# Optimization experiments

Hardware: AMD Instinct MI355X
Metric: run time of the kernel (lower is better)

The kernel has to match this reference:

```python
import jax, jax.numpy as jnp
import numpy as np

B, S, D, F_DIM, E, TOPK = 2, 1024, 1024, 4096, 8, 2


def setup_inputs() -> dict:
    key = jax.random.key(0)
    k0, k1, k2, k3 = jax.random.split(key, 4)
    hidden_states = jax.random.normal(k0, (B, S, D), dtype=jnp.float32)
    # torch nn.Linear stores weight as [out_features, in_features]
    router_w = jax.random.normal(k1, (E, D), dtype=jnp.float32) * 0.02
    w1 = jax.random.normal(k2, (E, F_DIM, D), dtype=jnp.float32) * 0.02
    w2 = jax.random.normal(k3, (E, D, F_DIM), dtype=jnp.float32) * 0.02
    expert_scale = jnp.ones((E,), dtype=jnp.float32)
    return {"hidden_states": hidden_states, "router_w": router_w,
            "w1": w1, "w2": w2, "expert_scale": expert_scale}


def reference(hidden_states, router_w, w1, w2, expert_scale):
    b, s, d = hidden_states.shape
    xf = hidden_states.reshape(-1, d)                      # [T, D]
    logits = xf @ router_w.T                               # [T, E]
    probs = jax.nn.softmax(logits, axis=-1)
    top_w, top_idx = jax.lax.top_k(probs, TOPK)            # [T, K]
    top_w = jax.nn.softmax(top_w, axis=-1)                 # renormalize over top-k
    # Combine weights per expert: sum of slot weights routed to each expert. [T, E]
    combine = jnp.sum(jax.nn.one_hot(top_idx, E, dtype=xf.dtype) * top_w[..., None], axis=1)
    # Dense per-expert SiLU MLP for all tokens (grouped GEMM form).
    h = jax.nn.silu(jnp.einsum('td,efd->tef', xf, w1))     # [T, E, F]
    y = jnp.einsum('tef,edf->ted', h, w2)                  # [T, E, D]
    y = y * expert_scale[None, :, None]
    out = jnp.einsum('te,ted->td', combine, y)             # [T, D]
    return out.reshape(b, s, d)
```

## Files before the change

kernel.cpp:

```cpp
#include <hip/hip_runtime.h>
#include <hip/hip_bf16.h>
#include <stdint.h>

#define NT 2048
#define DD 1024
#define FF 4096
#define NE 8
#define NSLOT (NT*2)

typedef float  f32x4  __attribute__((ext_vector_type(4)));
typedef __bf16 bf16x8 __attribute__((ext_vector_type(8)));
typedef __bf16 bf16x4 __attribute__((ext_vector_type(4)));

__global__ void k_convert_x(const float* __restrict__ x, __bf16* __restrict__ xb) {
    int i = blockIdx.x * blockDim.x + threadIdx.x;
    float4 v = reinterpret_cast<const float4*>(x)[i];
    bf16x4 o;
    o[0] = (__bf16)v.x; o[1] = (__bf16)v.y; o[2] = (__bf16)v.z; o[3] = (__bf16)v.w;
    reinterpret_cast<bf16x4*>(xb)[i] = o;
}

__global__ void k_router(const float* __restrict__ x, const float* __restrict__ rw,
                         const float* __restrict__ escale,
                         int* __restrict__ counts, int* __restrict__ rank,
                         int* __restrict__ tidx, float* __restrict__ tw) {
    int t = blockIdx.x;
    int lane = threadIdx.x;
    const float* xr = x + (size_t)t * DD + lane * 16;
    float acc[NE];
    #pragma unroll
    for (int e = 0; e < NE; e++) acc[e] = 0.f;
    #pragma unroll
    for (int c = 0; c < 4; c++) {
        float4 xv = reinterpret_cast<const float4*>(xr)[c];
        #pragma unroll
        for (int e = 0; e < NE; e++) {
            float4 rv = reinterpret_cast<const float4*>(rw + (size_t)e * DD + lane * 16)[c];
            acc[e] += xv.x*rv.x + xv.y*rv.y + xv.z*rv.z + xv.w*rv.w;
        }
    }
    #pragma unroll
    for (int e = 0; e < NE; e++) {
        #pragma unroll
        for (int off = 32; off > 0; off >>= 1) acc[e] += __shfl_xor(acc[e], off);
    }
    if (lane == 0) {
        int e0 = 0; float l0 = acc[0];
        #pragma unroll
        for (int e = 1; e < NE; e++) if (acc[e] > l0) { l0 = acc[e]; e0 = e; }
        int e1 = (e0 == 0) ? 1 : 0; float l1 = acc[e1];
        #pragma unroll
        for (int e = 0; e < NE; e++) if (e != e0 && acc[e] > l1) { l1 = acc[e]; e1 = e; }
        float sum = 0.f;
        #pragma unroll
        for (int e = 0; e < NE; e++) sum += __expf(acc[e] - l0);
        float p0 = 1.0f / sum;
        float p1 = __expf(l1 - l0) / sum;
        float z  = __expf(p1 - p0);
        float w0 = 1.0f / (1.0f + z);
        float w1 = 1.0f - w0;
        tidx[t*2+0] = e0; tw[t*2+0] = w0 * escale[e0];
        tidx[t*2+1] = e1; tw[t*2+1] = w1 * escale[e1];
        rank[t*2+0] = atomicAdd(&counts[e0], 1);
        rank[t*2+1] = atomicAdd(&counts[e1], 1);
    }
}

__global__ void k_prefix(const int* __restrict__ counts, int* __restrict__ offsets) {
    if (threadIdx.x == 0) {
        int s = 0;
        for (int e = 0; e < NE; e++) { offsets[e] = s; s += counts[e]; }
        offsets[NE] = s;
    }
}

__global__ void k_scatter(const int* __restrict__ tidx, const float* __restrict__ tw,
                          const int* __restrict__ rank, const int* __restrict__ offsets,
                          int* __restrict__ slot_token, int* __restrict__ slot_k,
                          float* __restrict__ slot_w) {
    int t = blockIdx.x * blockDim.x + threadIdx.x;
    if (t >= NT) return;
    #pragma unroll
    for (int k = 0; k < 2; k++) {
        int e = tidx[t*2+k];
        int p = offsets[e] + rank[t*2+k];
        slot_token[p] = t; slot_k[p] = k; slot_w[p] = tw[t*2+k];
    }
}

#define BM 128
#define BN 128
#define BK 32
#define LDT 40

__launch_bounds__(256)
__global__ void k_gemm1(const __bf16* __restrict__ xb, const float* __restrict__ w1,
                        const int* __restrict__ offsets, const int* __restrict__ slot_token,
                        __bf16* __restrict__ H) {
    int e = blockIdx.z;
    int base = offsets[e];
    int Me = offsets[e+1] - base;
    int m0 = blockIdx.x * BM;
    if (m0 >= Me) return;
    int n0 = blockIdx.y * BN;

    __shared__ __bf16 As[BM][LDT];
    __shared__ __bf16 Bs[BN][LDT];

    int tid = threadIdx.x;
    int wave = tid >> 6, lane = tid & 63;
    int wm = (wave & 1) * 64, wn = (wave >> 1) * 64;

    int arow = tid >> 1, ahalf = tid & 1;
    int rloc = min(m0 + arow, Me - 1);
    int tok  = slot_token[base + rloc];
    const __bf16* aptr = xb + (size_t)tok * DD + ahalf * 16;
    const float*  bptr = w1 + ((size_t)e * FF + n0 + arow) * DD + ahalf * 16;

    f32x4 zero4 = {0.f, 0.f, 0.f, 0.f};
    f32x4 acc[4][4];
    #pragma unroll
    for (int m = 0; m < 4; m++)
        #pragma unroll
        for (int n = 0; n < 4; n++) acc[m][n] = zero4;

    for (int k0 = 0; k0 < DD; k0 += BK) {
        const bf16x8* ap = reinterpret_cast<const bf16x8*>(aptr + k0);
        bf16x8 a0 = ap[0], a1 = ap[1];
        const float4* bp = reinterpret_cast<const float4*>(bptr + k0);
        float4 q0 = bp[0], q1 = bp[1], q2 = bp[2], q3 = bp[3];
        bf16x8 b0, b1;
        b0[0]=(__bf16)q0.x; b0[1]=(__bf16)q0.y; b0[2]=(__bf16)q0.z; b0[3]=(__bf16)q0.w;
        b0[4]=(__bf16)q1.x; b0[5]=(__bf16)q1.y; b0[6]=(__bf16)q1.z; b0[7]=(__bf16)q1.w;
        b1[0]=(__bf16)q2.x; b1[1]=(__bf16)q2.y; b1[2]=(__bf16)q2.z; b1[3]=(__bf16)q2.w;
        b1[4]=(__bf16)q3.x; b1[5]=(__bf16)q3.y; b1[6]=(__bf16)q3.z; b1[7]=(__bf16)q3.w;
        *reinterpret_cast<bf16x8*>(&As[arow][ahalf*16    ]) = a0;
        *reinterpret_cast<bf16x8*>(&As[arow][ahalf*16 + 8]) = a1;
        *reinterpret_cast<bf16x8*>(&Bs[arow][ahalf*16    ]) = b0;
        *reinterpret_cast<bf16x8*>(&Bs[arow][ahalf*16 + 8]) = b1;
        __syncthreads();
        bf16x8 af[4], bfr[4];
        #pragma unroll
        for (int m = 0; m < 4; m++)
            af[m] = *reinterpret_cast<const bf16x8*>(&As[wm + m*16 + (lane & 15)][(lane >> 4) * 8]);
        #pragma unroll
        for (int n = 0; n < 4; n++)
            bfr[n] = *reinterpret_cast<const bf16x8*>(&Bs[wn + n*16 + (lane & 15)][(lane >> 4) * 8]);
        #pragma unroll
        for (int m = 0; m < 4; m++)
            #pragma unroll
            for (int n = 0; n < 4; n++)
                acc[m][n] = __builtin_amdgcn_mfma_f32_16x16x32_bf16(af[m], bfr[n], acc[m][n], 0, 0, 0);
        __syncthreads();
    }

    int rbase = wm + (lane >> 4) * 4;
    int cbase = n0 + wn + (lane & 15);
    #pragma unroll
    for (int m = 0; m < 4; m++) {
        #pragma unroll
        for (int j = 0; j < 4; j++) {
            int rl = m0 + rbase + m*16 + j;
            if (rl < Me) {
                #pragma unroll
                for (int n = 0; n < 4; n++) {
                    float v = acc[m][n][j];
                    float s = v / (1.0f + __expf(-v));
                    H[(size_t)(base + rl) * FF + cbase + n*16] = (__bf16)s;
                }
            }
        }
    }
}

__launch_bounds__(256)
__global__ void k_gemm2(const __bf16* __restrict__ H, const float* __restrict__ w2,
                        const int* __restrict__ offsets,
                        const int* __restrict__ slot_token, const int* __restrict__ slot_k,
                        const float* __restrict__ slot_w,
                        float* __restrict__ ybuf) {
    int e = blockIdx.z;
    int base = offsets[e];
    int Me = offsets[e+1] - base;
    int m0 = blockIdx.x * BM;
    if (m0 >= Me) return;
    int n0 = blockIdx.y * BN;

    __shared__ __bf16 As[BM][LDT];
    __shared__ __bf16 Bs[BN][LDT];

    int tid = threadIdx.x;
    int wave = tid >> 6, lane = tid & 63;
    int wm = (wave & 1) * 64, wn = (wave >> 1) * 64;

    int arow = tid >> 1, ahalf = tid & 1;
    int rloc = min(m0 + arow, Me - 1);
    const __bf16* aptr = H  + (size_t)(base + rloc) * FF + ahalf * 16;
    const float*  bptr = w2 + ((size_t)e * DD + n0 + arow) * FF + ahalf * 16;

    f32x4 zero4 = {0.f, 0.f, 0.f, 0.f};
    f32x4 acc[4][4];
    #pragma unroll
    for (int m = 0; m < 4; m++)
        #pragma unroll
        for (int n = 0; n < 4; n++) acc[m][n] = zero4;

    for (int k0 = 0; k0 < FF; k0 += BK) {
        const bf16x8* ap = reinterpret_cast<const bf16x8*>(aptr + k0);
        bf16x8 a0 = ap[0], a1 = ap[1];
        const float4* bp = reinterpret_cast<const float4*>(bptr + k0);
        float4 q0 = bp[0], q1 = bp[1], q2 = bp[2], q3 = bp[3];
        bf16x8 b0, b1;
        b0[0]=(__bf16)q0.x; b0[1]=(__bf16)q0.y; b0[2]=(__bf16)q0.z; b0[3]=(__bf16)q0.w;
        b0[4]=(__bf16)q1.x; b0[5]=(__bf16)q1.y; b0[6]=(__bf16)q1.z; b0[7]=(__bf16)q1.w;
        b1[0]=(__bf16)q2.x; b1[1]=(__bf16)q2.y; b1[2]=(__bf16)q2.z; b1[3]=(__bf16)q2.w;
        b1[4]=(__bf16)q3.x; b1[5]=(__bf16)q3.y; b1[6]=(__bf16)q3.z; b1[7]=(__bf16)q3.w;
        *reinterpret_cast<bf16x8*>(&As[arow][ahalf*16    ]) = a0;
        *reinterpret_cast<bf16x8*>(&As[arow][ahalf*16 + 8]) = a1;
        *reinterpret_cast<bf16x8*>(&Bs[arow][ahalf*16    ]) = b0;
        *reinterpret_cast<bf16x8*>(&Bs[arow][ahalf*16 + 8]) = b1;
        __syncthreads();
        bf16x8 af[4], bfr[4];
        #pragma unroll
        for (int m = 0; m < 4; m++)
            af[m] = *reinterpret_cast<const bf16x8*>(&As[wm + m*16 + (lane & 15)][(lane >> 4) * 8]);
        #pragma unroll
        for (int n = 0; n < 4; n++)
            bfr[n] = *reinterpret_cast<const bf16x8*>(&Bs[wn + n*16 + (lane & 15)][(lane >> 4) * 8]);
        #pragma unroll
        for (int m = 0; m < 4; m++)
            #pragma unroll
            for (int n = 0; n < 4; n++)
                acc[m][n] = __builtin_amdgcn_mfma_f32_16x16x32_bf16(af[m], bfr[n], acc[m][n], 0, 0, 0);
        __syncthreads();
    }

    int rbase = wm + (lane >> 4) * 4;
    int cb = n0 + wn + (lane & 15);
    #pragma unroll
    for (int m = 0; m < 4; m++) {
        #pragma unroll
        for (int j = 0; j < 4; j++) {
            int rl = m0 + rbase + m*16 + j;
            if (rl < Me) {
                int p = base + rl;
                int tok = slot_token[p];
                int kk  = slot_k[p];
                float wv = slot_w[p];
                float* yrow = ybuf + ((size_t)tok * 2 + kk) * DD + cb;
                #pragma unroll
                for (int n = 0; n < 4; n++) yrow[n*16] = acc[m][n][j] * wv;
            }
        }
    }
}

__global__ void k_combine(const float* __restrict__ yb, float* __restrict__ out) {
    int i = blockIdx.x * blockDim.x + threadIdx.x;
    int t = i >> 8;
    int c = i & 255;
    const f32x4* a = reinterpret_cast<const f32x4*>(yb + (size_t)t * 2 * DD);
    f32x4 va = a[c];
    f32x4 vb = a[c + 256];
    reinterpret_cast<f32x4*>(out)[i] = va + vb;
}

extern "C" void kernel_launch(void* const* d_in, const int* in_sizes, int n_in,
                              void* d_out, int out_size, void* d_ws, size_t ws_size,
                              hipStream_t stream) {
    const float* x  = (const float*)d_in[0];
    const float* rw = (const float*)d_in[1];
    const float* w1 = (const float*)d_in[2];
    const float* w2 = (const float*)d_in[3];
    const float* es = (const float*)d_in[4];
    float* out = (float*)d_out;

    uint8_t* ws = (uint8_t*)d_ws;
    __bf16* xb   = (__bf16*)ws;  ws += (size_t)NT * DD * 2;
    __bf16* H    = (__bf16*)ws;  ws += (size_t)NSLOT * FF * 2;
    float*  ybuf = (float*)ws;   ws += (size_t)NT * 2 * DD * 4;
    int*    counts   = (int*)ws; ws += 64;
    int*    offsets  = (int*)ws; ws += 64;
    int*    tidx     = (int*)ws; ws += (size_t)NT * 2 * 4;
    float*  tw       = (float*)ws; ws += (size_t)NT * 2 * 4;
    int*    rank     = (int*)ws; ws += (size_t)NT * 2 * 4;
    int*    slot_token = (int*)ws; ws += (size_t)NSLOT * 4;
    int*    slot_k     = (int*)ws; ws += (size_t)NSLOT * 4;
    float*  slot_w     = (float*)ws; ws += (size_t)NSLOT * 4;

    hipMemsetAsync(counts, 0, NE * sizeof(int), stream);
    k_convert_x<<<NT * DD / 4 / 256, 256, 0, stream>>>(x, xb);
    k_router<<<NT, 64, 0, stream>>>(x, rw, es, counts, rank, tidx, tw);
    k_prefix<<<1, 1, 0, stream>>>(counts, offsets);
    k_scatter<<<NT / 256, 256, 0, stream>>>(tidx, tw, rank, offsets, slot_token, slot_k, slot_w);
    dim3 g1(NT / BM, FF / BN, NE);
    k_gemm1<<<g1, 256, 0, stream>>>(xb, w1, offsets, slot_token, H);
    dim3 g2(NT / BM, DD / BN, NE);
    k_gemm2<<<g2, 256, 0, stream>>>(H, w2, offsets, slot_token, slot_k, slot_w, ybuf);
    k_combine<<<NT * DD / 4 / 256, 256, 0, stream>>>(ybuf, out);
}
```

Before: 938.9 us.

## Use direct global-to-LDS loads, split-K second GEMM with atomic combine, fuse x conversion

Both grouped GEMMs now stage tiles with global_load_lds straight into shared memory, keeping the fp32 weights in LDS and converting them to bf16 when building fragments. The second GEMM is split along K into four chunks and accumulates the weighted results into the zeroed output with atomicAdd, which removes the ybuf intermediate and the combine kernel. The x-to-bf16 conversion is folded into the router kernel. In exchange, LDS traffic grows because fp32 B tiles are twice as large, atomic contention rises, and the floating-point sum order becomes nondeterministic.

```diff
diff --git a/kernel.cpp b/kernel.cpp
--- a/kernel.cpp
+++ b/kernel.cpp
@@ -12,31 +12,38 @@
 typedef __bf16 bf16x8 __attribute__((ext_vector_type(8)));
 typedef __bf16 bf16x4 __attribute__((ext_vector_type(4)));
 
-__global__ void k_convert_x(const float* __restrict__ x, __bf16* __restrict__ xb) {
-    int i = blockIdx.x * blockDim.x + threadIdx.x;
-    float4 v = reinterpret_cast<const float4*>(x)[i];
-    bf16x4 o;
-    o[0] = (__bf16)v.x; o[1] = (__bf16)v.y; o[2] = (__bf16)v.z; o[3] = (__bf16)v.w;
-    reinterpret_cast<bf16x4*>(xb)[i] = o;
+__device__ __forceinline__ void gl16(void* lds, const void* g) {
+    __builtin_amdgcn_global_load_lds(
+        (const __attribute__((address_space(1))) void*)g,
+        (__attribute__((address_space(3))) void*)lds, 16, 0, 0);
 }
 
 __global__ void k_router(const float* __restrict__ x, const float* __restrict__ rw,
-                         const float* __restrict__ escale,
+                         const float* __restrict__ escale, __bf16* __restrict__ xb,
                          int* __restrict__ counts, int* __restrict__ rank,
                          int* __restrict__ tidx, float* __restrict__ tw) {
     int t = blockIdx.x;
     int lane = threadIdx.x;
     const float* xr = x + (size_t)t * DD + lane * 16;
+    float4 xv[4];
+    #pragma unroll
+    for (int c = 0; c < 4; c++) xv[c] = reinterpret_cast<const float4*>(xr)[c];
+    #pragma unroll
+    for (int c = 0; c < 4; c++) {
+        bf16x4 o;
+        o[0] = (__bf16)xv[c].x; o[1] = (__bf16)xv[c].y;
+        o[2] = (__bf16)xv[c].z; o[3] = (__bf16)xv[c].w;
+        *reinterpret_cast<bf16x4*>(xb + (size_t)t * DD + lane * 16 + c * 4) = o;
+    }
     float acc[NE];
     #pragma unroll
     for (int e = 0; e < NE; e++) acc[e] = 0.f;
     #pragma unroll
     for (int c = 0; c < 4; c++) {
-        float4 xv = reinterpret_cast<const float4*>(xr)[c];
         #pragma unroll
         for (int e = 0; e < NE; e++) {
             float4 rv = reinterpret_cast<const float4*>(rw + (size_t)e * DD + lane * 16)[c];
-            acc[e] += xv.x*rv.x + xv.y*rv.y + xv.z*rv.z + xv.w*rv.w;
+            acc[e] += xv[c].x*rv.x + xv[c].y*rv.y + xv[c].z*rv.z + xv[c].w*rv.w;
         }
     }
     #pragma unroll
@@ -76,22 +83,21 @@
 
 __global__ void k_scatter(const int* __restrict__ tidx, const float* __restrict__ tw,
                           const int* __restrict__ rank, const int* __restrict__ offsets,
-                          int* __restrict__ slot_token, int* __restrict__ slot_k,
-                          float* __restrict__ slot_w) {
+                          int* __restrict__ slot_token, float* __restrict__ slot_w) {
     int t = blockIdx.x * blockDim.x + threadIdx.x;
     if (t >= NT) return;
     #pragma unroll
     for (int k = 0; k < 2; k++) {
         int e = tidx[t*2+k];
         int p = offsets[e] + rank[t*2+k];
-        slot_token[p] = t; slot_k[p] = k; slot_w[p] = tw[t*2+k];
+        slot_token[p] = t; slot_w[p] = tw[t*2+k];
     }
 }
 
 #define BM 128
 #define BN 128
 #define BK 32
-#define LDT 40
+#define KSPLIT 4
 
 __launch_bounds__(256)
 __global__ void k_gemm1(const __bf16* __restrict__ xb, const float* __restrict__ w1,
@@ -104,48 +110,53 @@
     if (m0 >= Me) return;
     int n0 = blockIdx.y * BN;
 
-    __shared__ __bf16 As[BM][LDT];
-    __shared__ __bf16 Bs[BN][LDT];
-
-    int tid = threadIdx.x;
-    int wave = tid >> 6, lane = tid & 63;
+    __shared__ __bf16 As[BM*BK];
+    __shared__ float  Bs[BN*BK];
+
+    int tid = threadIdx.x, wave = tid >> 6, lane = tid & 63;
     int wm = (wave & 1) * 64, wn = (wave >> 1) * 64;
 
-    int arow = tid >> 1, ahalf = tid & 1;
-    int rloc = min(m0 + arow, Me - 1);
-    int tok  = slot_token[base + rloc];
-    const __bf16* aptr = xb + (size_t)tok * DD + ahalf * 16;
-    const float*  bptr = w1 + ((size_t)e * FF + n0 + arow) * DD + ahalf * 16;
-
-    f32x4 zero4 = {0.f, 0.f, 0.f, 0.f};
+    const __bf16* aptr[2];
+    #pragma unroll
+    for (int j = 0; j < 2; j++) {
+        int r = (wave*2 + j) * 16 + (lane >> 2);
+        int rl = min(m0 + r, Me - 1);
+        int tok = slot_token[base + rl];
+        aptr[j] = xb + (size_t)tok * DD + (lane & 3) * 8;
+    }
+    const float* bptr[4];
+    #pragma unroll
+    for (int j = 0; j < 4; j++) {
+        int r = (wave*4 + j) * 8 + (lane >> 3);
+        bptr[j] = w1 + ((size_t)e * FF + n0 + r) * DD + (lane & 7) * 4;
+    }
+
     f32x4 acc[4][4];
     #pragma unroll
     for (int m = 0; m < 4; m++)
         #pragma unroll
-        for (int n = 0; n < 4; n++) acc[m][n] = zero4;
+        for (int n = 0; n < 4; n++) acc[m][n] = (f32x4){0.f,0.f,0.f,0.f};
 
     for (int k0 = 0; k0 < DD; k0 += BK) {
-        const bf16x8* ap = reinterpret_cast<const bf16x8*>(aptr + k0);
-        bf16x8 a0 = ap[0], a1 = ap[1];
-        const float4* bp = reinterpret_cast<const float4*>(bptr + k0);
-        float4 q0 = bp[0], q1 = bp[1], q2 = bp[2], q3 = bp[3];
-        bf16x8 b0, b1;
-        b0[0]=(__bf16)q0.x; b0[1]=(__bf16)q0.y; b0[2]=(__bf16)q0.z; b0[3]=(__bf16)q0.w;
-        b0[4]=(__bf16)q1.x; b0[5]=(__bf16)q1.y; b0[6]=(__bf16)q1.z; b0[7]=(__bf16)q1.w;
-        b1[0]=(__bf16)q2.x; b1[1]=(__bf16)q2.y; b1[2]=(__bf16)q2.z; b1[3]=(__bf16)q2.w;
-        b1[4]=(__bf16)q3.x; b1[5]=(__bf16)q3.y; b1[6]=(__bf16)q3.z; b1[7]=(__bf16)q3.w;
-        *reinterpret_cast<bf16x8*>(&As[arow][ahalf*16    ]) = a0;
-        *reinterpret_cast<bf16x8*>(&As[arow][ahalf*16 + 8]) = a1;
-        *reinterpret_cast<bf16x8*>(&Bs[arow][ahalf*16    ]) = b0;
-        *reinterpret_cast<bf16x8*>(&Bs[arow][ahalf*16 + 8]) = b1;
+        #pragma unroll
+        for (int j = 0; j < 2; j++) gl16(&As[(wave*2 + j) * 512], aptr[j] + k0);
+        #pragma unroll
+        for (int j = 0; j < 4; j++) gl16(&Bs[(wave*4 + j) * 256], bptr[j] + k0);
         __syncthreads();
         bf16x8 af[4], bfr[4];
         #pragma unroll
         for (int m = 0; m < 4; m++)
-            af[m] = *reinterpret_cast<const bf16x8*>(&As[wm + m*16 + (lane & 15)][(lane >> 4) * 8]);
-        #pragma unroll
-        for (int n = 0; n < 4; n++)
-            bfr[n] = *reinterpret_cast<const bf16x8*>(&Bs[wn + n*16 + (lane & 15)][(lane >> 4) * 8]);
+            af[m] = *reinterpret_cast<const bf16x8*>(&As[(wm + m*16 + (lane & 15)) * BK + (lane >> 4) * 8]);
+        #pragma unroll
+        for (int n = 0; n < 4; n++) {
+            const float* p = &Bs[(wn + n*16 + (lane & 15)) * BK + (lane >> 4) * 8];
+            float4 x0 = *reinterpret_cast<const float4*>(p);
+            float4 x1 = *reinterpret_cast<const float4*>(p + 4);
+            bf16x8 t;
+            t[0]=(__bf16)x0.x; t[1]=(__bf16)x0.y; t[2]=(__bf16)x0.z; t[3]=(__bf16)x0.w;
+            t[4]=(__bf16)x1.x; t[5]=(__bf16)x1.y; t[6]=(__bf16)x1.z; t[7]=(__bf16)x1.w;
+            bfr[n] = t;
+        }
         #pragma unroll
         for (int m = 0; m < 4; m++)
             #pragma unroll
@@ -176,57 +187,65 @@
 __launch_bounds__(256)
 __global__ void k_gemm2(const __bf16* __restrict__ H, const float* __restrict__ w2,
                         const int* __restrict__ offsets,
-                        const int* __restrict__ slot_token, const int* __restrict__ slot_k,
-                        const float* __restrict__ slot_w,
-                        float* __restrict__ ybuf) {
+                        const int* __restrict__ slot_token, const float* __restrict__ slot_w,
+                        float* __restrict__ out) {
     int e = blockIdx.z;
     int base = offsets[e];
     int Me = offsets[e+1] - base;
-    int m0 = blockIdx.x * BM;
+    int mt = blockIdx.x & 15;
+    int ch = blockIdx.x >> 4;
+    int m0 = mt * BM;
     if (m0 >= Me) return;
     int n0 = blockIdx.y * BN;
-
-    __shared__ __bf16 As[BM][LDT];
-    __shared__ __bf16 Bs[BN][LDT];
-
-    int tid = threadIdx.x;
-    int wave = tid >> 6, lane = tid & 63;
+    const int KCH = FF / KSPLIT;
+    int kbeg = ch * KCH;
+
+    __shared__ __bf16 As[BM*BK];
+    __shared__ float  Bs[BN*BK];
+
+    int tid = threadIdx.x, wave = tid >> 6, lane = tid & 63;
     int wm = (wave & 1) * 64, wn = (wave >> 1) * 64;
 
-    int arow = tid >> 1, ahalf = tid & 1;
-    int rloc = min(m0 + arow, Me - 1);
-    const __bf16* aptr = H  + (size_t)(base + rloc) * FF + ahalf * 16;
-    const float*  bptr = w2 + ((size_t)e * DD + n0 + arow) * FF + ahalf * 16;
-
-    f32x4 zero4 = {0.f, 0.f, 0.f, 0.f};
+    const __bf16* aptr[2];
+    #pragma unroll
+    for (int j = 0; j < 2; j++) {
+        int r = (wave*2 + j) * 16 + (lane >> 2);
+        int rl = min(m0 + r, Me - 1);
+        aptr[j] = H + (size_t)(base + rl) * FF + kbeg + (lane & 3) * 8;
+    }
+    const float* bptr[4];
+    #pragma unroll
+    for (int j = 0; j < 4; j++) {
+        int r = (wave*4 + j) * 8 + (lane >> 3);
+        bptr[j] = w2 + ((size_t)e * DD + n0 + r) * FF + kbeg + (lane & 7) * 4;
+    }
+
     f32x4 acc[4][4];
     #pragma unroll
     for (int m = 0; m < 4; m++)
         #pragma unroll
-        for (int n = 0; n < 4; n++) acc[m][n] = zero4;
-
-    for (int k0 = 0; k0 < FF; k0 += BK) {
-        const bf16x8* ap = reinterpret_cast<const bf16x8*>(aptr + k0);
-        bf16x8 a0 = ap[0], a1 = ap[1];
-        const float4* bp = reinterpret_cast<const float4*>(bptr + k0);
-        float4 q0 = bp[0], q1 = bp[1], q2 = bp[2], q3 = bp[3];
-        bf16x8 b0, b1;
-        b0[0]=(__bf16)q0.x; b0[1]=(__bf16)q0.y; b0[2]=(__bf16)q0.z; b0[3]=(__bf16)q0.w;
-        b0[4]=(__bf16)q1.x; b0[5]=(__bf16)q1.y; b0[6]=(__bf16)q1.z; b0[7]=(__bf16)q1.w;
-        b1[0]=(__bf16)q2.x; b1[1]=(__bf16)q2.y; b1[2]=(__bf16)q2.z; b1[3]=(__bf16)q2.w;
-        b1[4]=(__bf16)q3.x; b1[5]=(__bf16)q3.y; b1[6]=(__bf16)q3.z; b1[7]=(__bf16)q3.w;
-        *reinterpret_cast<bf16x8*>(&As[arow][ahalf*16    ]) = a0;
-        *reinterpret_cast<bf16x8*>(&As[arow][ahalf*16 + 8]) = a1;
-        *reinterpret_cast<bf16x8*>(&Bs[arow][ahalf*16    ]) = b0;
-        *reinterpret_cast<bf16x8*>(&Bs[arow][ahalf*16 + 8]) = b1;
+        for (int n = 0; n < 4; n++) acc[m][n] = (f32x4){0.f,0.f,0.f,0.f};
+
+    for (int k0 = 0; k0 < KCH; k0 += BK) {
+        #pragma unroll
+        for (int j = 0; j < 2; j++) gl16(&As[(wave*2 + j) * 512], aptr[j] + k0);
+        #pragma unroll
+        for (int j = 0; j < 4; j++) gl16(&Bs[(wave*4 + j) * 256], bptr[j] + k0);
         __syncthreads();
         bf16x8 af[4], bfr[4];
         #pragma unroll
         for (int m = 0; m < 4; m++)
-            af[m] = *reinterpret_cast<const bf16x8*>(&As[wm + m*16 + (lane & 15)][(lane >> 4) * 8]);
-        #pragma unroll
-        for (int n = 0; n < 4; n++)
-            bfr[n] = *reinterpret_cast<const bf16x8*>(&Bs[wn + n*16 + (lane & 15)][(lane >> 4) * 8]);
+            af[m] = *reinterpret_cast<const bf16x8*>(&As[(wm + m*16 + (lane & 15)) * BK + (lane >> 4) * 8]);
+        #pragma unroll
+        for (int n = 0; n < 4; n++) {
+            const float* p = &Bs[(wn + n*16 + (lane & 15)) * BK + (lane >> 4) * 8];
+            float4 x0 = *reinterpret_cast<const float4*>(p);
+            float4 x1 = *reinterpret_cast<const float4*>(p + 4);
+            bf16x8 t;
+            t[0]=(__bf16)x0.x; t[1]=(__bf16)x0.y; t[2]=(__bf16)x0.z; t[3]=(__bf16)x0.w;
+            t[4]=(__bf16)x1.x; t[5]=(__bf16)x1.y; t[6]=(__bf16)x1.z; t[7]=(__bf16)x1.w;
+            bfr[n] = t;
+        }
         #pragma unroll
         for (int m = 0; m < 4; m++)
             #pragma unroll
@@ -245,24 +264,14 @@
             if (rl < Me) {
                 int p = base + rl;
                 int tok = slot_token[p];
-                int kk  = slot_k[p];
                 float wv = slot_w[p];
-                float* yrow = ybuf + ((size_t)tok * 2 + kk) * DD + cb;
+                float* yrow = out + (size_t)tok * DD + cb;
                 #pragma unroll
-                for (int n = 0; n < 4; n++) yrow[n*16] = acc[m][n][j] * wv;
+                for (int n = 0; n < 4; n++)
+                    atomicAdd(&yrow[n*16], acc[m][n][j] * wv);
             }
         }
     }
-}
-
-__global__ void k_combine(const float* __restrict__ yb, float* __restrict__ out) {
-    int i = blockIdx.x * blockDim.x + threadIdx.x;
-    int t = i >> 8;
-    int c = i & 255;
-    const f32x4* a = reinterpret_cast<const f32x4*>(yb + (size_t)t * 2 * DD);
-    f32x4 va = a[c];
-    f32x4 vb = a[c + 256];
-    reinterpret_cast<f32x4*>(out)[i] = va + vb;
 }
 
 extern "C" void kernel_launch(void* const* d_in, const int* in_sizes, int n_in,
@@ -278,24 +287,21 @@
     uint8_t* ws = (uint8_t*)d_ws;
     __bf16* xb   = (__bf16*)ws;  ws += (size_t)NT * DD * 2;
     __bf16* H    = (__bf16*)ws;  ws += (size_t)NSLOT * FF * 2;
-    float*  ybuf = (float*)ws;   ws += (size_t)NT * 2 * DD * 4;
     int*    counts   = (int*)ws; ws += 64;
     int*    offsets  = (int*)ws; ws += 64;
     int*    tidx     = (int*)ws; ws += (size_t)NT * 2 * 4;
     float*  tw       = (float*)ws; ws += (size_t)NT * 2 * 4;
     int*    rank     = (int*)ws; ws += (size_t)NT * 2 * 4;
     int*    slot_token = (int*)ws; ws += (size_t)NSLOT * 4;
-    int*    slot_k     = (int*)ws; ws += (size_t)NSLOT * 4;
     float*  slot_w     = (float*)ws; ws += (size_t)NSLOT * 4;
 
     hipMemsetAsync(counts, 0, NE * sizeof(int), stream);
-    k_convert_x<<<NT * DD / 4 / 256, 256, 0, stream>>>(x, xb);
-    k_router<<<NT, 64, 0, stream>>>(x, rw, es, counts, rank, tidx, tw);
+    hipMemsetAsync(out, 0, (size_t)NT * DD * sizeof(float), stream);
+    k_router<<<NT, 64, 0, stream>>>(x, rw, es, xb, counts, rank, tidx, tw);
     k_prefix<<<1, 1, 0, stream>>>(counts, offsets);
-    k_scatter<<<NT / 256, 256, 0, stream>>>(tidx, tw, rank, offsets, slot_token, slot_k, slot_w);
+    k_scatter<<<NT / 256, 256, 0, stream>>>(tidx, tw, rank, offsets, slot_token, slot_w);
     dim3 g1(NT / BM, FF / BN, NE);
     k_gemm1<<<g1, 256, 0, stream>>>(xb, w1, offsets, slot_token, H);
-    dim3 g2(NT / BM, DD / BN, NE);
-    k_gemm2<<<g2, 256, 0, stream>>>(H, w2, offsets, slot_token, slot_k, slot_w, ybuf);
-    k_combine<<<NT * DD / 4 / 256, 256, 0, stream>>>(ybuf, out);
-}
+    dim3 g2((NT / BM) * KSPLIT, DD / BN, NE);
+    k_gemm2<<<g2, 256, 0, stream>>>(H, w2, offsets, slot_token, slot_w, out);
+}
```

Result: slower. 1.776 ms (+89.1%).
